# Performance work log

Measured on AMD Instinct MI355X. Metric: run time of the kernel, lower is better.

The kernel has to match this reference:

```python
import jax, jax.numpy as jnp
import numpy as np

B, S, E, HD = 8, 2048, 1024, 64  # batch, seq, n_embds, head_size (n_embds // n_heads)


def setup_inputs() -> dict:
    key = jax.random.key(0)
    k1, k2, k3, k4 = jax.random.split(key, 4)
    x = jax.random.normal(k1, (B, S, E), dtype=jnp.float32)
    # torch Linear weights have shape [out_features, in_features]; scale like default init
    Wk = jax.random.normal(k2, (HD, E), dtype=jnp.float32) * (1.0 / np.sqrt(E))
    Wq = jax.random.normal(k3, (HD, E), dtype=jnp.float32) * (1.0 / np.sqrt(E))
    Wv = jax.random.normal(k4, (HD, E), dtype=jnp.float32) * (1.0 / np.sqrt(E))
    return {"x": x, "Wk": Wk, "Wq": Wq, "Wv": Wv}


def reference(x, Wk, Wq, Wv):
    # q, k, v: [B, S, HD]
    k = jnp.einsum('bse,he->bsh', x, Wk)
    q = jnp.einsum('bse,he->bsh', x, Wq)
    v = jnp.einsum('bse,he->bsh', x, Wv)
    # scores: [B, S, S], scaled by sqrt(head_size)
    scores = jnp.einsum('bqh,bkh->bqk', q, k) / jnp.sqrt(jnp.float32(HD))
    # causal mask (tril): position q attends to k <= q
    causal = jnp.tril(jnp.ones((S, S), dtype=bool))
    scores = jnp.where(causal, scores, jnp.float32(-jnp.inf))
    attn = jax.nn.softmax(scores, axis=-1)
    # dropout_rate = 0.0 -> identity
    out = jnp.einsum('bqk,bkh->bqh', attn, v)  # [B, S, HD]
    return out
```

## Files before the change

kernel.cpp:

```cpp
#include <hip/hip_runtime.h>
#include <hip/hip_bf16.h>
#include <stdint.h>

typedef short bh8 __attribute__((ext_vector_type(8)));
typedef short bh4 __attribute__((ext_vector_type(4)));
typedef float fx4 __attribute__((ext_vector_type(4)));

#define B_ 8
#define S_ 2048
#define E_ 1024
#define HD_ 64

__device__ __forceinline__ short f2bf(float f) {
  unsigned u = __builtin_bit_cast(unsigned, f);
  u = u + 0x7FFFu + ((u >> 16) & 1u);
  return (short)(u >> 16);
}

#define GL2LDS16(gp, lp) __builtin_amdgcn_global_load_lds( \
    (const __attribute__((address_space(1))) unsigned int*)(gp), \
    (__attribute__((address_space(3))) unsigned int*)(lp), 16, 0, 0)


__global__ __launch_bounds__(256) void castw_k(
    const float* __restrict__ wk, const float* __restrict__ wq,
    const float* __restrict__ wv, short* __restrict__ wc) {
  int i = blockIdx.x * 256 + threadIdx.x;
  int wsel = i >> 13;
  int o = (i & 8191) * 8;
  const float* src = (wsel == 0) ? wk : (wsel == 1) ? wq : wv;
  float4 a = *(const float4*)(src + o);
  float4 b = *(const float4*)(src + o + 4);
  bh8 r = { f2bf(a.x), f2bf(a.y), f2bf(a.z), f2bf(a.w),
            f2bf(b.x), f2bf(b.y), f2bf(b.z), f2bf(b.w) };
  *(bh8*)(wc + wsel * (HD_ * E_) + o) = r;
}

__global__ __launch_bounds__(512) void qkv_gemm(
    const float* __restrict__ x, const short* __restrict__ wc,
    short* __restrict__ kfr, short* __restrict__ qfr, short* __restrict__ vfr) {
  __shared__ short As[2][32 * 32];
  __shared__ short Bs[2][192 * 32];
  const int tid = threadIdx.x;
  const int w = tid >> 6, l = tid & 63;
  const int c = l & 15, g = l >> 4;
  const int r0 = blockIdx.x * 32;
  const int wr = w & 1, wq = w >> 1;
  const int prow = l >> 2;
  const int pcol = (l & 3) * 8;
  const int at = tid - 256;
  const int ar = at >> 3;
  const int ac = (at & 7) * 4;
  const float* xrow = x + (size_t)(r0 + ar) * E_ + ac;

  fx4 acc[3];
  acc[0] = acc[1] = acc[2] = (fx4){0.f, 0.f, 0.f, 0.f};

  float4 xa;
  if (w < 4) {
    GL2LDS16(wc + (size_t)(16 * w + prow) * E_ + pcol, &Bs[0][w * 512]);
    GL2LDS16(wc + (size_t)(16 * (8 + w) + prow) * E_ + pcol, &Bs[0][(8 + w) * 512]);
  } else {
    GL2LDS16(wc + (size_t)(16 * w + prow) * E_ + pcol, &Bs[0][w * 512]);
    xa = *(const float4*)(xrow);
    bh4 aw = { f2bf(xa.x), f2bf(xa.y), f2bf(xa.z), f2bf(xa.w) };
    *(bh4*)&As[0][ar * 32 + ac] = aw;
    __builtin_amdgcn_sched_barrier(0);
    xa = *(const float4*)(xrow + 32);
  }
  __builtin_amdgcn_sched_barrier(0);
  if (w < 4) { asm volatile("s_waitcnt vmcnt(0) lgkmcnt(0)" ::: "memory"); }
  else       { asm volatile("s_waitcnt vmcnt(1) lgkmcnt(0)" ::: "memory"); }
  __builtin_amdgcn_s_barrier();
  __builtin_amdgcn_sched_barrier(0);

  for (int t = 0; t < 32; ++t) {
    const int cur = t & 1;
    if (t < 31) {
      const int k1 = (t + 1) * 32;
      if (w < 4) {
        GL2LDS16(wc + (size_t)(16 * w + prow) * E_ + k1 + pcol, &Bs[cur ^ 1][w * 512]);
        GL2LDS16(wc + (size_t)(16 * (8 + w) + prow) * E_ + k1 + pcol, &Bs[cur ^ 1][(8 + w) * 512]);
      } else {
        GL2LDS16(wc + (size_t)(16 * w + prow) * E_ + k1 + pcol, &Bs[cur ^ 1][w * 512]);
        bh4 aw = { f2bf(xa.x), f2bf(xa.y), f2bf(xa.z), f2bf(xa.w) };
        *(bh4*)&As[cur ^ 1][ar * 32 + ac] = aw;
        __builtin_amdgcn_sched_barrier(0);
        const int k2 = (t + 2 < 32) ? (t + 2) * 32 : 0;
        xa = *(const float4*)(xrow + k2);
      }
      __builtin_amdgcn_sched_barrier(0);
    }

    bh8 af = *(const bh8*)&As[cur][(16 * wr + c) * 32 + 8 * g];
#pragma unroll
    for (int cc = 0; cc < 3; ++cc) {
      bh8 bf = *(const bh8*)&Bs[cur][(16 * (3 * wq + cc) + c) * 32 + 8 * g];
      acc[cc] = __builtin_amdgcn_mfma_f32_16x16x32_bf16(af, bf, acc[cc], 0, 0, 0);
    }

    if (t < 31) {
      __builtin_amdgcn_sched_barrier(0);
      if (w < 4) { asm volatile("s_waitcnt vmcnt(0) lgkmcnt(0)" ::: "memory"); }
      else       { asm volatile("s_waitcnt vmcnt(1) lgkmcnt(0)" ::: "memory"); }
      __builtin_amdgcn_s_barrier();
      __builtin_amdgcn_sched_barrier(0);
    }
  }

  const int rbase = r0 + 16 * wr + 4 * g;
  const int bb = rbase >> 11;
  const int srw = rbase & (S_ - 1);
  const int kt = srw >> 4;
  const int g2 = (srw & 15) >> 2;
#pragma unroll
  for (int cc = 0; cc < 3; ++cc) {
    const int ctg = 3 * wq + cc;
    const int n = 16 * ctg + c;
    if (ctg < 4) {
      const int h = n >> 5, gg = (n & 31) >> 3, jj = n & 7;
      short* dst = kfr + ((size_t)(((bb * 128 + kt) * 2 + h) * 64 + gg * 16) * 8) + jj;
#pragma unroll
      for (int j = 0; j < 4; ++j)
        dst[(size_t)(((rbase + j) & 15)) * 8] = f2bf(acc[cc][j]);
    } else if (ctg < 8) {
      const int nq = n - 64;
      const int h = nq >> 5, gg = (nq & 31) >> 3, jj = nq & 7;
      short* dst = qfr + ((size_t)(((bb * 128 + kt) * 2 + h) * 64 + gg * 16) * 8) + jj;
#pragma unroll
      for (int j = 0; j < 4; ++j)
        dst[(size_t)(((rbase + j) & 15)) * 8] = f2bf(acc[cc][j] * 0.125f);
    } else {
      const int hd = n - 128;
      const int mm = hd >> 4, c2 = hd & 15;
      bh4 pk = { f2bf(acc[cc][0]), f2bf(acc[cc][1]),
                 f2bf(acc[cc][2]), f2bf(acc[cc][3]) };
      *(bh4*)&vfr[(size_t)(((bb * 128 + kt) * 4 + mm) * 64 + g2 * 16 + c2) * 4] = pk;
    }
  }
}

__global__ __launch_bounds__(512, 4) void attn_fused3(
    const short* __restrict__ qfr, const short* __restrict__ kfr,
    const short* __restrict__ vfr, float* __restrict__ out) {
  __shared__ float sO[8][16][68];
  __shared__ float sL[8][16];
  const int tid = threadIdx.x;
  const int w = tid >> 6, l = tid & 63;
  const int c = l & 15, g = l >> 4;
  const int b = blockIdx.x >> 6, p = blockIdx.x & 63;
  const int qtA = p, qtB = 127 - p;

  const short* qbB = qfr + (size_t)(b * 128) * 1024;
  const short* kbB = kfr + (size_t)(b * 128) * 1024;
  const short* vbB = vfr + (size_t)(b * 128) * 1024;

  bh8 qA0 = *(const bh8*)(qbB + (qtA * 2 + 0) * 512 + l * 8);
  bh8 qA1 = *(const bh8*)(qbB + (qtA * 2 + 1) * 512 + l * 8);
  bh8 qB0 = *(const bh8*)(qbB + (qtB * 2 + 0) * 512 + l * 8);
  bh8 qB1 = *(const bh8*)(qbB + (qtB * 2 + 1) * 512 + l * 8);

  fx4 oA[4], oB[4];
#pragma unroll
  for (int mm = 0; mm < 4; ++mm) { oA[mm] = (fx4){0,0,0,0}; oB[mm] = (fx4){0,0,0,0}; }
  float lA = 0.f, lB = 0.f;

  for (int kt = w; kt <= qtB; kt += 8) {
    const short* kp = kbB + kt * 1024;
    bh8 kf0 = *(const bh8*)(kp + l * 8);
    bh8 kf1 = *(const bh8*)(kp + 512 + l * 8);
    const short* vp = vbB + kt * 1024;
    bh4 vf0 = *(const bh4*)(vp + l * 4);
    bh4 vf1 = *(const bh4*)(vp + 256 + l * 4);
    bh4 vf2 = *(const bh4*)(vp + 512 + l * 4);
    bh4 vf3 = *(const bh4*)(vp + 768 + l * 4);

    fx4 sB = {0.f, 0.f, 0.f, 0.f};
    sB = __builtin_amdgcn_mfma_f32_16x16x32_bf16(kf0, qB0, sB, 0, 0, 0);
    sB = __builtin_amdgcn_mfma_f32_16x16x32_bf16(kf1, qB1, sB, 0, 0, 0);
    if (kt == qtB) {
#pragma unroll
      for (int j = 0; j < 4; ++j)
        if (4 * g + j > c) sB[j] = -1e30f;
    }
    const float pB0 = __expf(sB[0] - 8.f);
    const float pB1 = __expf(sB[1] - 8.f);
    const float pB2 = __expf(sB[2] - 8.f);
    const float pB3 = __expf(sB[3] - 8.f);
    lB += (pB0 + pB1) + (pB2 + pB3);
    bh4 pfB = { f2bf(pB0), f2bf(pB1), f2bf(pB2), f2bf(pB3) };
    oB[0] = __builtin_amdgcn_mfma_f32_16x16x16bf16_1k(vf0, pfB, oB[0], 0, 0, 0);
    oB[1] = __builtin_amdgcn_mfma_f32_16x16x16bf16_1k(vf1, pfB, oB[1], 0, 0, 0);
    oB[2] = __builtin_amdgcn_mfma_f32_16x16x16bf16_1k(vf2, pfB, oB[2], 0, 0, 0);
    oB[3] = __builtin_amdgcn_mfma_f32_16x16x16bf16_1k(vf3, pfB, oB[3], 0, 0, 0);

    if (kt <= qtA) {
      fx4 sA = {0.f, 0.f, 0.f, 0.f};
      sA = __builtin_amdgcn_mfma_f32_16x16x32_bf16(kf0, qA0, sA, 0, 0, 0);
      sA = __builtin_amdgcn_mfma_f32_16x16x32_bf16(kf1, qA1, sA, 0, 0, 0);
      if (kt == qtA) {
#pragma unroll
        for (int j = 0; j < 4; ++j)
          if (4 * g + j > c) sA[j] = -1e30f;
      }
      const float pA0 = __expf(sA[0] - 8.f);
      const float pA1 = __expf(sA[1] - 8.f);
      const float pA2 = __expf(sA[2] - 8.f);
      const float pA3 = __expf(sA[3] - 8.f);
      lA += (pA0 + pA1) + (pA2 + pA3);
      bh4 pfA = { f2bf(pA0), f2bf(pA1), f2bf(pA2), f2bf(pA3) };
      oA[0] = __builtin_amdgcn_mfma_f32_16x16x16bf16_1k(vf0, pfA, oA[0], 0, 0, 0);
      oA[1] = __builtin_amdgcn_mfma_f32_16x16x16bf16_1k(vf1, pfA, oA[1], 0, 0, 0);
      oA[2] = __builtin_amdgcn_mfma_f32_16x16x16bf16_1k(vf2, pfA, oA[2], 0, 0, 0);
      oA[3] = __builtin_amdgcn_mfma_f32_16x16x16bf16_1k(vf3, pfA, oA[3], 0, 0, 0);
    }
  }

#pragma unroll
  for (int mm = 0; mm < 4; ++mm)
    *(fx4*)&sO[w][c][16 * mm + 4 * g] = oA[mm];
  lA += __shfl_xor(lA, 16, 64);
  lA += __shfl_xor(lA, 32, 64);
  if (g == 0) sL[w][c] = lA;
  __syncthreads();
  if (w < 4) {
    const int r = tid >> 4;
    const int cg4 = (tid & 15) * 4;
    fx4 a = {0.f, 0.f, 0.f, 0.f};
    float L = 0.f;
#pragma unroll
    for (int i = 0; i < 8; ++i) { a += *(const fx4*)&sO[i][r][cg4]; L += sL[i][r]; }
    fx4 res = a * (1.0f / L);
    *(fx4*)(out + ((size_t)(b * S_ + qtA * 16 + r)) * HD_ + cg4) = res;
  }
  __syncthreads();
#pragma unroll
  for (int mm = 0; mm < 4; ++mm)
    *(fx4*)&sO[w][c][16 * mm + 4 * g] = oB[mm];
  lB += __shfl_xor(lB, 16, 64);
  lB += __shfl_xor(lB, 32, 64);
  if (g == 0) sL[w][c] = lB;
  __syncthreads();
  if (w < 4) {
    const int r = tid >> 4;
    const int cg4 = (tid & 15) * 4;
    fx4 a = {0.f, 0.f, 0.f, 0.f};
    float L = 0.f;
#pragma unroll
    for (int i = 0; i < 8; ++i) { a += *(const fx4*)&sO[i][r][cg4]; L += sL[i][r]; }
    fx4 res = a * (1.0f / L);
    *(fx4*)(out + ((size_t)(b * S_ + qtB * 16 + r)) * HD_ + cg4) = res;
  }
}

extern "C" void kernel_launch(void* const* d_in, const int* in_sizes, int n_in,
                              void* d_out, int out_size, void* d_ws, size_t ws_size,
                              hipStream_t stream) {
  const float* x  = (const float*)d_in[0];
  const float* wk = (const float*)d_in[1];
  const float* wq = (const float*)d_in[2];
  const float* wv = (const float*)d_in[3];
  float* out = (float*)d_out;
  char* ws = (char*)d_ws;
  short* wc  = (short*)(ws);
  short* kfr = (short*)(ws + 393216);
  short* qfr = (short*)(ws + 2490368);
  short* vfr = (short*)(ws + 4587520);

  castw_k<<<dim3(96), dim3(256), 0, stream>>>(wk, wq, wv, wc);
  qkv_gemm<<<dim3(512), dim3(512), 0, stream>>>(x, wc, kfr, qfr, vfr);
  attn_fused3<<<dim3(512), dim3(512), 0, stream>>>(qfr, kfr, vfr, out);
}
```

Baseline: 48.91 us.

## Double-buffer K/V tiles into LDS via async global-to-LDS loads per wave

Each wave now prefetches the next K/V tile into a private double-buffered LDS region with global_load_lds, while it computes on the current tile. Previously K/V fragments were loaded from global memory straight into registers right before use. The aim is to hide global load latency behind the MFMA and exp work. The cost is 64KB of LDS per block, which limits occupancy, plus a full vmcnt(0) wait every iteration and an extra LDS read. The launch-bounds occupancy hint is also dropped.

```diff
diff --git a/kernel.cpp b/kernel.cpp
--- a/kernel.cpp
+++ b/kernel.cpp
@@ -140,11 +140,10 @@
   }
 }
 
-__global__ __launch_bounds__(512, 4) void attn_fused3(
+__global__ __launch_bounds__(512) void attn_fused4(
     const short* __restrict__ qfr, const short* __restrict__ kfr,
     const short* __restrict__ vfr, float* __restrict__ out) {
-  __shared__ float sO[8][16][68];
-  __shared__ float sL[8][16];
+  __shared__ short smem[32768];
   const int tid = threadIdx.x;
   const int w = tid >> 6, l = tid & 63;
   const int c = l & 15, g = l >> 4;
@@ -154,6 +153,7 @@
   const short* qbB = qfr + (size_t)(b * 128) * 1024;
   const short* kbB = kfr + (size_t)(b * 128) * 1024;
   const short* vbB = vfr + (size_t)(b * 128) * 1024;
+  short* kv = smem + w * 4096;
 
   bh8 qA0 = *(const bh8*)(qbB + (qtA * 2 + 0) * 512 + l * 8);
   bh8 qA1 = *(const bh8*)(qbB + (qtA * 2 + 1) * 512 + l * 8);
@@ -165,15 +165,30 @@
   for (int mm = 0; mm < 4; ++mm) { oA[mm] = (fx4){0,0,0,0}; oB[mm] = (fx4){0,0,0,0}; }
   float lA = 0.f, lB = 0.f;
 
+#define STAGEKV(dstbuf, T) \
+  GL2LDS16(kbB + (size_t)(T) * 1024 + l * 8,        kv + (dstbuf) * 2048); \
+  GL2LDS16(kbB + (size_t)(T) * 1024 + 512 + l * 8,  kv + (dstbuf) * 2048 + 512); \
+  GL2LDS16(vbB + (size_t)(T) * 1024 + l * 8,        kv + (dstbuf) * 2048 + 1024); \
+  GL2LDS16(vbB + (size_t)(T) * 1024 + 512 + l * 8,  kv + (dstbuf) * 2048 + 1536);
+
+  STAGEKV(0, w)
+  __builtin_amdgcn_sched_barrier(0);
+  asm volatile("s_waitcnt vmcnt(0)" ::: "memory");
+  __builtin_amdgcn_sched_barrier(0);
+
+  int buf = 0;
   for (int kt = w; kt <= qtB; kt += 8) {
-    const short* kp = kbB + kt * 1024;
-    bh8 kf0 = *(const bh8*)(kp + l * 8);
-    bh8 kf1 = *(const bh8*)(kp + 512 + l * 8);
-    const short* vp = vbB + kt * 1024;
-    bh4 vf0 = *(const bh4*)(vp + l * 4);
-    bh4 vf1 = *(const bh4*)(vp + 256 + l * 4);
-    bh4 vf2 = *(const bh4*)(vp + 512 + l * 4);
-    bh4 vf3 = *(const bh4*)(vp + 768 + l * 4);
+    const int ktn = (kt + 8 <= qtB) ? kt + 8 : kt;
+    STAGEKV(buf ^ 1, ktn)
+    __builtin_amdgcn_sched_barrier(0);
+
+    const short* kb_ = kv + buf * 2048;
+    bh8 kf0 = *(const bh8*)(kb_ + l * 8);
+    bh8 kf1 = *(const bh8*)(kb_ + 512 + l * 8);
+    bh4 vf0 = *(const bh4*)(kb_ + 1024 + l * 4);
+    bh4 vf1 = *(const bh4*)(kb_ + 1024 + 256 + l * 4);
+    bh4 vf2 = *(const bh4*)(kb_ + 1024 + 512 + l * 4);
+    bh4 vf3 = *(const bh4*)(kb_ + 1024 + 768 + l * 4);
 
     fx4 sB = {0.f, 0.f, 0.f, 0.f};
     sB = __builtin_amdgcn_mfma_f32_16x16x32_bf16(kf0, qB0, sB, 0, 0, 0);
@@ -214,14 +229,25 @@
       oA[2] = __builtin_amdgcn_mfma_f32_16x16x16bf16_1k(vf2, pfA, oA[2], 0, 0, 0);
       oA[3] = __builtin_amdgcn_mfma_f32_16x16x16bf16_1k(vf3, pfA, oA[3], 0, 0, 0);
     }
-  }
+
+    __builtin_amdgcn_sched_barrier(0);
+    asm volatile("s_waitcnt vmcnt(0)" ::: "memory");
+    __builtin_amdgcn_sched_barrier(0);
+    buf ^= 1;
+  }
+#undef STAGEKV
+
+  __syncthreads();
+
+  float* sOf = (float*)smem;
+  float* sLf = sOf + 8 * 16 * 68;
 
 #pragma unroll
   for (int mm = 0; mm < 4; ++mm)
-    *(fx4*)&sO[w][c][16 * mm + 4 * g] = oA[mm];
+    *(fx4*)&sOf[(w * 16 + c) * 68 + 16 * mm + 4 * g] = oA[mm];
   lA += __shfl_xor(lA, 16, 64);
   lA += __shfl_xor(lA, 32, 64);
-  if (g == 0) sL[w][c] = lA;
+  if (g == 0) sLf[w * 16 + c] = lA;
   __syncthreads();
   if (w < 4) {
     const int r = tid >> 4;
@@ -229,17 +255,17 @@
     fx4 a = {0.f, 0.f, 0.f, 0.f};
     float L = 0.f;
 #pragma unroll
-    for (int i = 0; i < 8; ++i) { a += *(const fx4*)&sO[i][r][cg4]; L += sL[i][r]; }
+    for (int i = 0; i < 8; ++i) { a += *(const fx4*)&sOf[(i * 16 + r) * 68 + cg4]; L += sLf[i * 16 + r]; }
     fx4 res = a * (1.0f / L);
     *(fx4*)(out + ((size_t)(b * S_ + qtA * 16 + r)) * HD_ + cg4) = res;
   }
   __syncthreads();
 #pragma unroll
   for (int mm = 0; mm < 4; ++mm)
-    *(fx4*)&sO[w][c][16 * mm + 4 * g] = oB[mm];
+    *(fx4*)&sOf[(w * 16 + c) * 68 + 16 * mm + 4 * g] = oB[mm];
   lB += __shfl_xor(lB, 16, 64);
   lB += __shfl_xor(lB, 32, 64);
-  if (g == 0) sL[w][c] = lB;
+  if (g == 0) sLf[w * 16 + c] = lB;
   __syncthreads();
   if (w < 4) {
     const int r = tid >> 4;
@@ -247,7 +273,7 @@
     fx4 a = {0.f, 0.f, 0.f, 0.f};
     float L = 0.f;
 #pragma unroll
-    for (int i = 0; i < 8; ++i) { a += *(const fx4*)&sO[i][r][cg4]; L += sL[i][r]; }
+    for (int i = 0; i < 8; ++i) { a += *(const fx4*)&sOf[(i * 16 + r) * 68 + cg4]; L += sLf[i * 16 + r]; }
     fx4 res = a * (1.0f / L);
     *(fx4*)(out + ((size_t)(b * S_ + qtB * 16 + r)) * HD_ + cg4) = res;
   }
@@ -269,5 +295,5 @@
 
   castw_k<<<dim3(96), dim3(256), 0, stream>>>(wk, wq, wv, wc);
   qkv_gemm<<<dim3(512), dim3(512), 0, stream>>>(x, wc, kfr, qfr, vfr);
-  attn_fused3<<<dim3(512), dim3(512), 0, stream>>>(qfr, kfr, vfr, out);
-}
+  attn_fused4<<<dim3(512), dim3(512), 0, stream>>>(qfr, kfr, vfr, out);
+}
```

New measurement: 49.14 us. About the same (+0.5%).

## Split QKV projection GEMM along K into two halves with combine pass

Applied to the files above, without the earlier changes.

The QKV projection GEMM is split along the reduction dimension into two halves, doubling the grid from 512 to 1024 blocks. Each half writes bf16 partial results to a separate workspace region, and a new combine kernel adds the two partials and rounds back to bf16. The aim is more parallelism and better CU occupancy in the projection stage. The cost is an extra kernel launch, extra global traffic for the partials, and an additional bf16 rounding step on the partial sums.

```diff
diff --git a/kernel.cpp b/kernel.cpp
--- a/kernel.cpp
+++ b/kernel.cpp
@@ -15,6 +15,10 @@
   unsigned u = __builtin_bit_cast(unsigned, f);
   u = u + 0x7FFFu + ((u >> 16) & 1u);
   return (short)(u >> 16);
+}
+__device__ __forceinline__ float bf2f(short s) {
+  unsigned u = ((unsigned)(unsigned short)s) << 16;
+  return __builtin_bit_cast(float, u);
 }
 
 #define GL2LDS16(gp, lp) __builtin_amdgcn_global_load_lds( \
@@ -38,30 +42,37 @@
 
 __global__ __launch_bounds__(512) void qkv_gemm(
     const float* __restrict__ x, const short* __restrict__ wc,
-    short* __restrict__ kfr, short* __restrict__ qfr, short* __restrict__ vfr) {
+    short* __restrict__ pf) {
   __shared__ short As[2][32 * 32];
   __shared__ short Bs[2][192 * 32];
   const int tid = threadIdx.x;
   const int w = tid >> 6, l = tid & 63;
   const int c = l & 15, g = l >> 4;
-  const int r0 = blockIdx.x * 32;
+  const int rb = blockIdx.x & 511;
+  const int kh = blockIdx.x >> 9;
+  const int r0 = rb * 32;
+  const int kb0 = kh * 512;
   const int wr = w & 1, wq = w >> 1;
   const int prow = l >> 2;
   const int pcol = (l & 3) * 8;
   const int at = tid - 256;
   const int ar = at >> 3;
   const int ac = (at & 7) * 4;
-  const float* xrow = x + (size_t)(r0 + ar) * E_ + ac;
+  const float* xrow = x + (size_t)(r0 + ar) * E_ + kb0 + ac;
+
+  short* kfp = pf + (size_t)kh * 3145728;
+  short* qfp = kfp + 1048576;
+  short* vfp = kfp + 2097152;
 
   fx4 acc[3];
   acc[0] = acc[1] = acc[2] = (fx4){0.f, 0.f, 0.f, 0.f};
 
   float4 xa;
   if (w < 4) {
-    GL2LDS16(wc + (size_t)(16 * w + prow) * E_ + pcol, &Bs[0][w * 512]);
-    GL2LDS16(wc + (size_t)(16 * (8 + w) + prow) * E_ + pcol, &Bs[0][(8 + w) * 512]);
+    GL2LDS16(wc + (size_t)(16 * w + prow) * E_ + kb0 + pcol, &Bs[0][w * 512]);
+    GL2LDS16(wc + (size_t)(16 * (8 + w) + prow) * E_ + kb0 + pcol, &Bs[0][(8 + w) * 512]);
   } else {
-    GL2LDS16(wc + (size_t)(16 * w + prow) * E_ + pcol, &Bs[0][w * 512]);
+    GL2LDS16(wc + (size_t)(16 * w + prow) * E_ + kb0 + pcol, &Bs[0][w * 512]);
     xa = *(const float4*)(xrow);
     bh4 aw = { f2bf(xa.x), f2bf(xa.y), f2bf(xa.z), f2bf(xa.w) };
     *(bh4*)&As[0][ar * 32 + ac] = aw;
@@ -74,10 +85,10 @@
   __builtin_amdgcn_s_barrier();
   __builtin_amdgcn_sched_barrier(0);
 
-  for (int t = 0; t < 32; ++t) {
+  for (int t = 0; t < 16; ++t) {
     const int cur = t & 1;
-    if (t < 31) {
-      const int k1 = (t + 1) * 32;
+    if (t < 15) {
+      const int k1 = kb0 + (t + 1) * 32;
       if (w < 4) {
         GL2LDS16(wc + (size_t)(16 * w + prow) * E_ + k1 + pcol, &Bs[cur ^ 1][w * 512]);
         GL2LDS16(wc + (size_t)(16 * (8 + w) + prow) * E_ + k1 + pcol, &Bs[cur ^ 1][(8 + w) * 512]);
@@ -86,7 +97,7 @@
         bh4 aw = { f2bf(xa.x), f2bf(xa.y), f2bf(xa.z), f2bf(xa.w) };
         *(bh4*)&As[cur ^ 1][ar * 32 + ac] = aw;
         __builtin_amdgcn_sched_barrier(0);
-        const int k2 = (t + 2 < 32) ? (t + 2) * 32 : 0;
+        const int k2 = (t + 2 < 16) ? (t + 2) * 32 : 0;
         xa = *(const float4*)(xrow + k2);
       }
       __builtin_amdgcn_sched_barrier(0);
@@ -99,7 +110,7 @@
       acc[cc] = __builtin_amdgcn_mfma_f32_16x16x32_bf16(af, bf, acc[cc], 0, 0, 0);
     }
 
-    if (t < 31) {
+    if (t < 15) {
       __builtin_amdgcn_sched_barrier(0);
       if (w < 4) { asm volatile("s_waitcnt vmcnt(0) lgkmcnt(0)" ::: "memory"); }
       else       { asm volatile("s_waitcnt vmcnt(1) lgkmcnt(0)" ::: "memory"); }
@@ -119,14 +130,14 @@
     const int n = 16 * ctg + c;
     if (ctg < 4) {
       const int h = n >> 5, gg = (n & 31) >> 3, jj = n & 7;
-      short* dst = kfr + ((size_t)(((bb * 128 + kt) * 2 + h) * 64 + gg * 16) * 8) + jj;
+      short* dst = kfp + ((size_t)(((bb * 128 + kt) * 2 + h) * 64 + gg * 16) * 8) + jj;
 #pragma unroll
       for (int j = 0; j < 4; ++j)
         dst[(size_t)(((rbase + j) & 15)) * 8] = f2bf(acc[cc][j]);
     } else if (ctg < 8) {
       const int nq = n - 64;
       const int h = nq >> 5, gg = (nq & 31) >> 3, jj = nq & 7;
-      short* dst = qfr + ((size_t)(((bb * 128 + kt) * 2 + h) * 64 + gg * 16) * 8) + jj;
+      short* dst = qfp + ((size_t)(((bb * 128 + kt) * 2 + h) * 64 + gg * 16) * 8) + jj;
 #pragma unroll
       for (int j = 0; j < 4; ++j)
         dst[(size_t)(((rbase + j) & 15)) * 8] = f2bf(acc[cc][j] * 0.125f);
@@ -135,9 +146,26 @@
       const int mm = hd >> 4, c2 = hd & 15;
       bh4 pk = { f2bf(acc[cc][0]), f2bf(acc[cc][1]),
                  f2bf(acc[cc][2]), f2bf(acc[cc][3]) };
-      *(bh4*)&vfr[(size_t)(((bb * 128 + kt) * 4 + mm) * 64 + g2 * 16 + c2) * 4] = pk;
-    }
-  }
+      *(bh4*)&vfp[(size_t)(((bb * 128 + kt) * 4 + mm) * 64 + g2 * 16 + c2) * 4] = pk;
+    }
+  }
+}
+
+__global__ __launch_bounds__(256) void combine_k(
+    const short* __restrict__ pf, short* __restrict__ kqv) {
+  const size_t i = ((size_t)blockIdx.x * 256 + threadIdx.x) * 16;
+  bh8 a0 = *(const bh8*)(pf + i);
+  bh8 a1 = *(const bh8*)(pf + i + 8);
+  bh8 b0 = *(const bh8*)(pf + 3145728 + i);
+  bh8 b1 = *(const bh8*)(pf + 3145728 + i + 8);
+  bh8 r0, r1;
+#pragma unroll
+  for (int j = 0; j < 8; ++j) {
+    r0[j] = f2bf(bf2f(a0[j]) + bf2f(b0[j]));
+    r1[j] = f2bf(bf2f(a1[j]) + bf2f(b1[j]));
+  }
+  *(bh8*)(kqv + i) = r0;
+  *(bh8*)(kqv + i + 8) = r1;
 }
 
 __global__ __launch_bounds__(512, 4) void attn_fused3(
@@ -263,11 +291,13 @@
   float* out = (float*)d_out;
   char* ws = (char*)d_ws;
   short* wc  = (short*)(ws);
-  short* kfr = (short*)(ws + 393216);
-  short* qfr = (short*)(ws + 2490368);
-  short* vfr = (short*)(ws + 4587520);
-
+  short* kqv = (short*)(ws + 393216);
+  short* kfr = kqv;
+  short* qfr = kqv + 1048576;
+  short* vfr = kqv + 2097152;
+  short* pf  = (short*)(ws + 6684672);
   castw_k<<<dim3(96), dim3(256), 0, stream>>>(wk, wq, wv, wc);
-  qkv_gemm<<<dim3(512), dim3(512), 0, stream>>>(x, wc, kfr, qfr, vfr);
+  qkv_gemm<<<dim3(1024), dim3(512), 0, stream>>>(x, wc, pf);
+  combine_k<<<dim3(768), dim3(256), 0, stream>>>(pf, kqv);
   attn_fused3<<<dim3(512), dim3(512), 0, stream>>>(qfr, kfr, vfr, out);
 }
```

Measured after the change: 51.31 us. 1.05x slower.

## Process four query tiles per attention block to reuse K/V fragment loads

Applied to the files above, without the earlier changes.

The attention kernel now assigns four 16-row query tiles to each block instead of two: two adjacent low tiles paired with two adjacent high tiles, so the causal work stays balanced. Each K/V fragment loaded per iteration feeds up to four QK/PV MFMA chains, which halves the global K/V traffic per unit of work. The grid shrinks from 512 to 256 blocks and launch bounds drop to 2 blocks per CU to leave room for the extra registers. The costs are lower occupancy, only 256 blocks on the device, and a longer serialized epilogue with four merge passes.

```diff
diff --git a/kernel.cpp b/kernel.cpp
--- a/kernel.cpp
+++ b/kernel.cpp
@@ -140,7 +140,7 @@
   }
 }
 
-__global__ __launch_bounds__(512, 4) void attn_fused3(
+__global__ __launch_bounds__(512, 2) void attn_fused5(
     const short* __restrict__ qfr, const short* __restrict__ kfr,
     const short* __restrict__ vfr, float* __restrict__ out) {
   __shared__ float sO[8][16][68];
@@ -148,24 +148,53 @@
   const int tid = threadIdx.x;
   const int w = tid >> 6, l = tid & 63;
   const int c = l & 15, g = l >> 4;
-  const int b = blockIdx.x >> 6, p = blockIdx.x & 63;
-  const int qtA = p, qtB = 127 - p;
+  const int b = blockIdx.x >> 5, p = blockIdx.x & 31;
+  const int qt0 = 2 * p, qt1 = 2 * p + 1, qt2 = 126 - 2 * p, qt3 = 127 - 2 * p;
 
   const short* qbB = qfr + (size_t)(b * 128) * 1024;
   const short* kbB = kfr + (size_t)(b * 128) * 1024;
   const short* vbB = vfr + (size_t)(b * 128) * 1024;
 
-  bh8 qA0 = *(const bh8*)(qbB + (qtA * 2 + 0) * 512 + l * 8);
-  bh8 qA1 = *(const bh8*)(qbB + (qtA * 2 + 1) * 512 + l * 8);
-  bh8 qB0 = *(const bh8*)(qbB + (qtB * 2 + 0) * 512 + l * 8);
-  bh8 qB1 = *(const bh8*)(qbB + (qtB * 2 + 1) * 512 + l * 8);
-
-  fx4 oA[4], oB[4];
-#pragma unroll
-  for (int mm = 0; mm < 4; ++mm) { oA[mm] = (fx4){0,0,0,0}; oB[mm] = (fx4){0,0,0,0}; }
-  float lA = 0.f, lB = 0.f;
-
-  for (int kt = w; kt <= qtB; kt += 8) {
+  bh8 q0a = *(const bh8*)(qbB + (qt0 * 2 + 0) * 512 + l * 8);
+  bh8 q0b = *(const bh8*)(qbB + (qt0 * 2 + 1) * 512 + l * 8);
+  bh8 q1a = *(const bh8*)(qbB + (qt1 * 2 + 0) * 512 + l * 8);
+  bh8 q1b = *(const bh8*)(qbB + (qt1 * 2 + 1) * 512 + l * 8);
+  bh8 q2a = *(const bh8*)(qbB + (qt2 * 2 + 0) * 512 + l * 8);
+  bh8 q2b = *(const bh8*)(qbB + (qt2 * 2 + 1) * 512 + l * 8);
+  bh8 q3a = *(const bh8*)(qbB + (qt3 * 2 + 0) * 512 + l * 8);
+  bh8 q3b = *(const bh8*)(qbB + (qt3 * 2 + 1) * 512 + l * 8);
+
+  fx4 o0[4], o1[4], o2[4], o3[4];
+#pragma unroll
+  for (int mm = 0; mm < 4; ++mm) {
+    o0[mm] = (fx4){0,0,0,0}; o1[mm] = (fx4){0,0,0,0};
+    o2[mm] = (fx4){0,0,0,0}; o3[mm] = (fx4){0,0,0,0};
+  }
+  float l0 = 0.f, l1 = 0.f, l2 = 0.f, l3 = 0.f;
+
+#define QSTEP(QA, QB, OO, LS, QT) \
+  if (kt <= (QT)) { \
+    fx4 s = {0.f, 0.f, 0.f, 0.f}; \
+    s = __builtin_amdgcn_mfma_f32_16x16x32_bf16(kf0, QA, s, 0, 0, 0); \
+    s = __builtin_amdgcn_mfma_f32_16x16x32_bf16(kf1, QB, s, 0, 0, 0); \
+    if (kt == (QT)) { \
+      _Pragma("unroll") \
+      for (int j = 0; j < 4; ++j) \
+        if (4 * g + j > c) s[j] = -1e30f; \
+    } \
+    const float e0 = __expf(s[0] - 8.f); \
+    const float e1 = __expf(s[1] - 8.f); \
+    const float e2 = __expf(s[2] - 8.f); \
+    const float e3 = __expf(s[3] - 8.f); \
+    LS += (e0 + e1) + (e2 + e3); \
+    bh4 pf = { f2bf(e0), f2bf(e1), f2bf(e2), f2bf(e3) }; \
+    OO[0] = __builtin_amdgcn_mfma_f32_16x16x16bf16_1k(vf0, pf, OO[0], 0, 0, 0); \
+    OO[1] = __builtin_amdgcn_mfma_f32_16x16x16bf16_1k(vf1, pf, OO[1], 0, 0, 0); \
+    OO[2] = __builtin_amdgcn_mfma_f32_16x16x16bf16_1k(vf2, pf, OO[2], 0, 0, 0); \
+    OO[3] = __builtin_amdgcn_mfma_f32_16x16x16bf16_1k(vf3, pf, OO[3], 0, 0, 0); \
+  }
+
+  for (int kt = w; kt <= qt3; kt += 8) {
     const short* kp = kbB + kt * 1024;
     bh8 kf0 = *(const bh8*)(kp + l * 8);
     bh8 kf1 = *(const bh8*)(kp + 512 + l * 8);
@@ -175,82 +204,40 @@
     bh4 vf2 = *(const bh4*)(vp + 512 + l * 4);
     bh4 vf3 = *(const bh4*)(vp + 768 + l * 4);
 
-    fx4 sB = {0.f, 0.f, 0.f, 0.f};
-    sB = __builtin_amdgcn_mfma_f32_16x16x32_bf16(kf0, qB0, sB, 0, 0, 0);
-    sB = __builtin_amdgcn_mfma_f32_16x16x32_bf16(kf1, qB1, sB, 0, 0, 0);
-    if (kt == qtB) {
-#pragma unroll
-      for (int j = 0; j < 4; ++j)
-        if (4 * g + j > c) sB[j] = -1e30f;
-    }
-    const float pB0 = __expf(sB[0] - 8.f);
-    const float pB1 = __expf(sB[1] - 8.f);
-    const float pB2 = __expf(sB[2] - 8.f);
-    const float pB3 = __expf(sB[3] - 8.f);
-    lB += (pB0 + pB1) + (pB2 + pB3);
-    bh4 pfB = { f2bf(pB0), f2bf(pB1), f2bf(pB2), f2bf(pB3) };
-    oB[0] = __builtin_amdgcn_mfma_f32_16x16x16bf16_1k(vf0, pfB, oB[0], 0, 0, 0);
-    oB[1] = __builtin_amdgcn_mfma_f32_16x16x16bf16_1k(vf1, pfB, oB[1], 0, 0, 0);
-    oB[2] = __builtin_amdgcn_mfma_f32_16x16x16bf16_1k(vf2, pfB, oB[2], 0, 0, 0);
-    oB[3] = __builtin_amdgcn_mfma_f32_16x16x16bf16_1k(vf3, pfB, oB[3], 0, 0, 0);
-
-    if (kt <= qtA) {
-      fx4 sA = {0.f, 0.f, 0.f, 0.f};
-      sA = __builtin_amdgcn_mfma_f32_16x16x32_bf16(kf0, qA0, sA, 0, 0, 0);
-      sA = __builtin_amdgcn_mfma_f32_16x16x32_bf16(kf1, qA1, sA, 0, 0, 0);
-      if (kt == qtA) {
-#pragma unroll
-        for (int j = 0; j < 4; ++j)
-          if (4 * g + j > c) sA[j] = -1e30f;
-      }
-      const float pA0 = __expf(sA[0] - 8.f);
-      const float pA1 = __expf(sA[1] - 8.f);
-      const float pA2 = __expf(sA[2] - 8.f);
-      const float pA3 = __expf(sA[3] - 8.f);
-      lA += (pA0 + pA1) + (pA2 + pA3);
-      bh4 pfA = { f2bf(pA0), f2bf(pA1), f2bf(pA2), f2bf(pA3) };
-      oA[0] = __builtin_amdgcn_mfma_f32_16x16x16bf16_1k(vf0, pfA, oA[0], 0, 0, 0);
-      oA[1] = __builtin_amdgcn_mfma_f32_16x16x16bf16_1k(vf1, pfA, oA[1], 0, 0, 0);
-      oA[2] = __builtin_amdgcn_mfma_f32_16x16x16bf16_1k(vf2, pfA, oA[2], 0, 0, 0);
-      oA[3] = __builtin_amdgcn_mfma_f32_16x16x16bf16_1k(vf3, pfA, oA[3], 0, 0, 0);
-    }
-  }
-
-#pragma unroll
-  for (int mm = 0; mm < 4; ++mm)
-    *(fx4*)&sO[w][c][16 * mm + 4 * g] = oA[mm];
-  lA += __shfl_xor(lA, 16, 64);
-  lA += __shfl_xor(lA, 32, 64);
-  if (g == 0) sL[w][c] = lA;
-  __syncthreads();
-  if (w < 4) {
-    const int r = tid >> 4;
-    const int cg4 = (tid & 15) * 4;
-    fx4 a = {0.f, 0.f, 0.f, 0.f};
-    float L = 0.f;
-#pragma unroll
-    for (int i = 0; i < 8; ++i) { a += *(const fx4*)&sO[i][r][cg4]; L += sL[i][r]; }
-    fx4 res = a * (1.0f / L);
-    *(fx4*)(out + ((size_t)(b * S_ + qtA * 16 + r)) * HD_ + cg4) = res;
-  }
-  __syncthreads();
-#pragma unroll
-  for (int mm = 0; mm < 4; ++mm)
-    *(fx4*)&sO[w][c][16 * mm + 4 * g] = oB[mm];
-  lB += __shfl_xor(lB, 16, 64);
-  lB += __shfl_xor(lB, 32, 64);
-  if (g == 0) sL[w][c] = lB;
-  __syncthreads();
-  if (w < 4) {
-    const int r = tid >> 4;
-    const int cg4 = (tid & 15) * 4;
-    fx4 a = {0.f, 0.f, 0.f, 0.f};
-    float L = 0.f;
-#pragma unroll
-    for (int i = 0; i < 8; ++i) { a += *(const fx4*)&sO[i][r][cg4]; L += sL[i][r]; }
-    fx4 res = a * (1.0f / L);
-    *(fx4*)(out + ((size_t)(b * S_ + qtB * 16 + r)) * HD_ + cg4) = res;
-  }
+    QSTEP(q3a, q3b, o3, l3, qt3)
+    QSTEP(q2a, q2b, o2, l2, qt2)
+    QSTEP(q1a, q1b, o1, l1, qt1)
+    QSTEP(q0a, q0b, o0, l0, qt0)
+  }
+#undef QSTEP
+
+#define MERGE(OO, LS, QT) \
+  { \
+    _Pragma("unroll") \
+    for (int mm = 0; mm < 4; ++mm) \
+      *(fx4*)&sO[w][c][16 * mm + 4 * g] = OO[mm]; \
+    LS += __shfl_xor(LS, 16, 64); \
+    LS += __shfl_xor(LS, 32, 64); \
+    if (g == 0) sL[w][c] = LS; \
+    __syncthreads(); \
+    if (w < 4) { \
+      const int r = tid >> 4; \
+      const int cg4 = (tid & 15) * 4; \
+      fx4 a = {0.f, 0.f, 0.f, 0.f}; \
+      float L = 0.f; \
+      _Pragma("unroll") \
+      for (int i = 0; i < 8; ++i) { a += *(const fx4*)&sO[i][r][cg4]; L += sL[i][r]; } \
+      fx4 res = a * (1.0f / L); \
+      *(fx4*)(out + ((size_t)(b * S_ + (QT) * 16 + r)) * HD_ + cg4) = res; \
+    } \
+    __syncthreads(); \
+  }
+
+  MERGE(o0, l0, qt0)
+  MERGE(o1, l1, qt1)
+  MERGE(o2, l2, qt2)
+  MERGE(o3, l3, qt3)
+#undef MERGE
 }
 
 extern "C" void kernel_launch(void* const* d_in, const int* in_sizes, int n_in,
@@ -269,5 +256,5 @@
 
   castw_k<<<dim3(96), dim3(256), 0, stream>>>(wk, wq, wv, wc);
   qkv_gemm<<<dim3(512), dim3(512), 0, stream>>>(x, wc, kfr, qfr, vfr);
-  attn_fused3<<<dim3(512), dim3(512), 0, stream>>>(qfr, kfr, vfr, out);
-}
+  attn_fused5<<<dim3(256), dim3(512), 0, stream>>>(qfr, kfr, vfr, out);
+}
```

Result: slower. 51.32 us (+4.9%).
